# Optimization experiments

Hardware: AMD Instinct MI355X
Metric: run time of the kernel (lower is better)

Reference implementation:

```python
import jax, jax.numpy as jnp
import numpy as np

T, M = 8192, 64  # timesteps, number of correlated series


def setup_inputs() -> dict:
    key = jax.random.key(0)
    k_y, k_mu, k_sig = jax.random.split(key, 3)
    y = jax.random.normal(k_y, (T, M), dtype=jnp.float32)
    MU = (jax.random.normal(k_mu, (M,), dtype=jnp.float32) * 0.01)
    sigma0 = jax.random.uniform(k_sig, (M,), dtype=jnp.float32, minval=0.5, maxval=1.5)
    alpha0 = sigma0  # ctor initializes alpha0 = std(y,0) as well
    alpha = jnp.full((M,), 0.25, dtype=jnp.float32)
    beta = jnp.full((M,), 0.25, dtype=jnp.float32)
    # L0 = cholesky of a correlation matrix (ctor uses corrcoef(y.T))
    rng = np.random.default_rng(0)
    Z = rng.standard_normal((M, 4 * M)).astype(np.float64)
    C = Z @ Z.T
    d = np.sqrt(np.diag(C))
    C = C / np.outer(d, d)
    L0 = jnp.asarray(np.linalg.cholesky(C), dtype=jnp.float32)
    A = jnp.full((1,), 0.9, dtype=jnp.float32)
    B = jnp.full((1,), 0.05, dtype=jnp.float32)
    return dict(y=y, MU=MU, sigma0=sigma0, alpha0=alpha0, alpha=alpha,
                beta=beta, L0=L0, A=A, B=B)


def reference(y, MU, sigma0, alpha0, alpha, beta, L0, A, B):
    """DCC-GARCH conditional moments.
    Returns (mus [T,M], Sigmas [T,M,M]) — the parameters of the
    MultivariateNormalFullCovariance the TF model constructs.
    """
    n = y.shape[1]
    A0 = L0.T @ L0                  # unconditional correlation target (M,M)
    a0 = alpha0 ** 2                # (M,)

    def step(carry, y_t):
        u, sig, Q = carry           # u:(M,), sig:(M,), Q:(M,M)
        sig_t = jnp.sqrt(a0 + alpha * sig ** 2 + beta * u ** 2)
        ustd = u / sig
        Psi = jnp.outer(ustd, ustd)
        Q_t = A0 + A * (Q - A0) + B * (Psi - A0)
        dinv = 1.0 / jnp.sqrt(jnp.diagonal(Q_t))
        R_t = Q_t * jnp.outer(dinv, dinv)        # cov_to_corr
        Sigma_t = R_t * jnp.outer(sig_t, sig_t)  # D_t @ R_t @ D_t
        return (y_t - MU, sig_t, Q_t), Sigma_t

    u0 = jnp.zeros((n,), dtype=y.dtype)
    _, Sigmas = jax.lax.scan(step, (u0, sigma0, A0), y)
    mus = jnp.broadcast_to(MU, y.shape)
    return mus, Sigmas
```

## Files before the change

kernel.cpp:

```cpp
#include <hip/hip_runtime.h>
#include <hip/hip_bf16.h>
#include <stdint.h>

#define TT 8192
#define MM 64
#define CHUNK 32
#define WQ 48
#define WS 16
#define YROWS (CHUNK + WQ + WS)
#define NSPLIT 4

typedef float f4 __attribute__((ext_vector_type(4)));

__global__ __launch_bounds__(256, 4)
void dcc_kernel(const float* __restrict__ y, const float* __restrict__ MU,
                const float* __restrict__ sigma0, const float* __restrict__ alpha0,
                const float* __restrict__ alpha, const float* __restrict__ beta,
                const float* __restrict__ L0, const float* __restrict__ Ap,
                const float* __restrict__ Bp,
                float* __restrict__ out)
{
    __shared__ float lds_yu[YROWS][MM];
    __shared__ float lds_s[CHUNK][MM];

    const int tid  = threadIdx.x;
    const int chnk = blockIdx.x >> 2;
    const int h    = blockIdx.x & 3;
    const int c0   = chnk * CHUNK;
    const int cend = c0 + CHUNK;
    const int tq0  = (c0 > WQ) ? (c0 - WQ) : 0;
    const int ts0  = (tq0 > WS) ? (tq0 - WS) : 0;

    const float A = Ap[0], B = Bp[0];
    const float kappa = 1.0f - A - B;

    float* out_mu = out;
    float* out_sg = out + (size_t)TT * MM;

    if (h == 0) {
        int o = tid * 8;
        int m = o & (MM - 1);
        f4 a = *(const f4*)(MU + m);
        f4 b = *(const f4*)(MU + m + 4);
        float* dst = out_mu + (size_t)c0 * MM + o;
        __builtin_nontemporal_store(a, (f4*)(dst));
        __builtin_nontemporal_store(b, (f4*)(dst + 4));
    }

    {
        const float* ysrc = y + (size_t)ts0 * MM;
        const int nflt = (cend - ts0) * MM;
        for (int o = tid * 4; o < nflt; o += 256 * 4) {
            f4 v = *(const f4*)(ysrc + o);
            *(f4*)(&lds_yu[0][0] + o) = v;
        }
    }
    __syncthreads();

    if (tid < MM) {
        const int m = tid;
        const float mu  = MU[m];
        const float al  = alpha[m], be = beta[m];
        const float a0v = alpha0[m] * alpha0[m];
        float s2 = sigma0[m] * sigma0[m];
        float u_prev = (ts0 > 0) ? (y[(size_t)(ts0 - 1) * MM + m] - mu) : 0.0f;
        for (int t = ts0; t < cend; ++t) {
            float yt  = lds_yu[t - ts0][m];
            float s2n = fmaf(al, s2, fmaf(be, u_prev * u_prev, a0v));
            if (t >= tq0) lds_yu[t - tq0][m] = u_prev * rsqrtf(s2);
            if (t >= c0)  lds_s[t - c0][m]   = sqrtf(s2n);
            u_prev = yt - mu;
            s2 = s2n;
        }
    }

    const int j0 = (tid & 15) * 4;
    const int i0 = h * 16 + (tid >> 4);

    float acc[4], adr = 0.f, adc[4];
    #pragma unroll
    for (int b = 0; b < 4; ++b) { acc[b] = 0.f; adc[b] = 0.f; }

    #pragma unroll 4
    for (int k = 0; k < MM; ++k) {
        float li = L0[k * MM + i0];
        f4 Lj = *(const f4*)(L0 + k * MM + j0);
        float lj[4] = {Lj.x, Lj.y, Lj.z, Lj.w};
        #pragma unroll
        for (int b = 0; b < 4; ++b) {
            acc[b] = fmaf(li, lj[b], acc[b]);
            adc[b] = fmaf(lj[b], lj[b], adc[b]);
        }
        adr = fmaf(li, li, adr);
    }
    __syncthreads();

    float q[4], Cm[4], qdc[4], Cdc[4];
    float qdr = adr, Cdr = kappa * adr;
    #pragma unroll
    for (int b = 0; b < 4; ++b) {
        q[b]   = acc[b];
        Cm[b]  = kappa * acc[b];
        qdc[b] = adc[b];
        Cdc[b] = kappa * adc[b];
    }

    for (int t = tq0; t < cend; ++t) {
        const int r = t - tq0;
        float ui = lds_yu[r][i0];
        f4 U_j = *(const f4*)(&lds_yu[r][j0]);
        float uj[4] = {U_j.x, U_j.y, U_j.z, U_j.w};
        float bui = B * ui;
        #pragma unroll
        for (int b = 0; b < 4; ++b) {
            q[b] = fmaf(A, q[b], fmaf(bui, uj[b], Cm[b]));
            float buj = B * uj[b];
            qdc[b] = fmaf(A, qdc[b], fmaf(buj, uj[b], Cdc[b]));
        }
        qdr = fmaf(A, qdr, fmaf(bui, ui, Cdr));
        if (t >= c0) {
            float si = lds_s[t - c0][i0];
            f4 S_j = *(const f4*)(&lds_s[t - c0][j0]);
            float f = si * rsqrtf(qdr);
            float rj[4] = { S_j.x * rsqrtf(qdc[0]), S_j.y * rsqrtf(qdc[1]),
                            S_j.z * rsqrtf(qdc[2]), S_j.w * rsqrtf(qdc[3]) };
            f4 w;
            w.x = q[0] * f * rj[0];
            w.y = q[1] * f * rj[1];
            w.z = q[2] * f * rj[2];
            w.w = q[3] * f * rj[3];
            float* o = out_sg + ((size_t)t << 12) + (i0 << 6) + j0;
            __builtin_nontemporal_store(w, (f4*)o);
        }
    }
}

extern "C" void kernel_launch(void* const* d_in, const int* in_sizes, int n_in,
                              void* d_out, int out_size, void* d_ws, size_t ws_size,
                              hipStream_t stream) {
    (void)in_sizes; (void)n_in; (void)out_size; (void)d_ws; (void)ws_size;
    const float* y      = (const float*)d_in[0];
    const float* MU     = (const float*)d_in[1];
    const float* sigma0 = (const float*)d_in[2];
    const float* alpha0 = (const float*)d_in[3];
    const float* alpha  = (const float*)d_in[4];
    const float* beta   = (const float*)d_in[5];
    const float* L0     = (const float*)d_in[6];
    const float* A      = (const float*)d_in[7];
    const float* B      = (const float*)d_in[8];
    dcc_kernel<<<dim3((TT / CHUNK) * NSPLIT), dim3(256), 0, stream>>>(
        y, MU, sigma0, alpha0, alpha, beta, L0, A, B, (float*)d_out);
}
```

Measured before the change: 180.5 us.

## Split DCC into state kernel and output kernel via workspace buffers

Splits the single fused kernel into two launches. The first computes per-series standardized residuals and a combined scale factor (sigma times the inverse sqrt of the Q diagonal) into workspace, plus L0^T L0 once. The second recomputes only the off-diagonal Q recurrence per chunk and writes Sigma. This removes the redundant 4x recomputation of the variance scan, the L0 product and the diagonal Q recurrences in every block, and doubles the chunk size to amortize warm-up. In exchange it adds a second launch, workspace round-trips, and switches from nontemporal to regular stores.

```diff
diff --git a/kernel.cpp b/kernel.cpp
--- a/kernel.cpp
+++ b/kernel.cpp
@@ -1,59 +1,76 @@
 #include <hip/hip_runtime.h>
-#include <hip/hip_bf16.h>
 #include <stdint.h>
 
 #define TT 8192
 #define MM 64
-#define CHUNK 32
-#define WQ 48
-#define WS 16
-#define YROWS (CHUNK + WQ + WS)
+#define ACH 32
+#define AWQ 48
+#define AWS 16
+#define AROWS (ACH + AWQ + AWS)
+#define BCH 64
+#define BWQ 48
+#define BROWS (BCH + BWQ)
 #define NSPLIT 4
 
 typedef float f4 __attribute__((ext_vector_type(4)));
 
-__global__ __launch_bounds__(256, 4)
-void dcc_kernel(const float* __restrict__ y, const float* __restrict__ MU,
-                const float* __restrict__ sigma0, const float* __restrict__ alpha0,
-                const float* __restrict__ alpha, const float* __restrict__ beta,
-                const float* __restrict__ L0, const float* __restrict__ Ap,
-                const float* __restrict__ Bp,
-                float* __restrict__ out)
+__global__ __launch_bounds__(256, 2)
+void dcc_state(const float* __restrict__ y, const float* __restrict__ MU,
+               const float* __restrict__ sigma0, const float* __restrict__ alpha0,
+               const float* __restrict__ alpha, const float* __restrict__ beta,
+               const float* __restrict__ L0, const float* __restrict__ Ap,
+               const float* __restrict__ Bp,
+               float* __restrict__ out_mu, float* __restrict__ ustd_ws,
+               float* __restrict__ g_ws, float* __restrict__ a0_ws)
 {
-    __shared__ float lds_yu[YROWS][MM];
-    __shared__ float lds_s[CHUNK][MM];
-
-    const int tid  = threadIdx.x;
-    const int chnk = blockIdx.x >> 2;
-    const int h    = blockIdx.x & 3;
-    const int c0   = chnk * CHUNK;
-    const int cend = c0 + CHUNK;
-    const int tq0  = (c0 > WQ) ? (c0 - WQ) : 0;
-    const int ts0  = (tq0 > WS) ? (tq0 - WS) : 0;
-
+    const int tid = threadIdx.x;
+    const int blk = blockIdx.x;
     const float A = Ap[0], B = Bp[0];
     const float kappa = 1.0f - A - B;
 
-    float* out_mu = out;
-    float* out_sg = out + (size_t)TT * MM;
-
-    if (h == 0) {
+    if (blk == TT / ACH) {
+        const int i  = tid >> 2;
+        const int j0 = (tid & 3) * 16;
+        float acc[16];
+        #pragma unroll
+        for (int b = 0; b < 16; ++b) acc[b] = 0.f;
+        for (int k = 0; k < MM; ++k) {
+            float li = L0[k * MM + i];
+            const float* row = L0 + k * MM + j0;
+            #pragma unroll
+            for (int b = 0; b < 16; ++b)
+                acc[b] = fmaf(li, row[b], acc[b]);
+        }
+        #pragma unroll
+        for (int b = 0; b < 16; b += 4) {
+            f4 w = {acc[b], acc[b + 1], acc[b + 2], acc[b + 3]};
+            *(f4*)(a0_ws + i * MM + j0 + b) = w;
+        }
+        return;
+    }
+
+    __shared__ float lds_y[AROWS][MM];
+
+    const int c0   = blk * ACH;
+    const int cend = c0 + ACH;
+    const int tq0  = (c0 > AWQ) ? c0 - AWQ : 0;
+    const int ts0  = (tq0 > AWS) ? tq0 - AWS : 0;
+
+    {
         int o = tid * 8;
         int m = o & (MM - 1);
         f4 a = *(const f4*)(MU + m);
         f4 b = *(const f4*)(MU + m + 4);
         float* dst = out_mu + (size_t)c0 * MM + o;
-        __builtin_nontemporal_store(a, (f4*)(dst));
-        __builtin_nontemporal_store(b, (f4*)(dst + 4));
+        *(f4*)dst       = a;
+        *(f4*)(dst + 4) = b;
     }
 
     {
         const float* ysrc = y + (size_t)ts0 * MM;
         const int nflt = (cend - ts0) * MM;
-        for (int o = tid * 4; o < nflt; o += 256 * 4) {
-            f4 v = *(const f4*)(ysrc + o);
-            *(f4*)(&lds_yu[0][0] + o) = v;
-        }
+        for (int o = tid * 4; o < nflt; o += 1024)
+            *(f4*)(&lds_y[0][0] + o) = *(const f4*)(ysrc + o);
     }
     __syncthreads();
 
@@ -62,83 +79,104 @@
         const float mu  = MU[m];
         const float al  = alpha[m], be = beta[m];
         const float a0v = alpha0[m] * alpha0[m];
+        float adm = 0.f;
+        for (int k = 0; k < MM; ++k) {
+            float l = L0[k * MM + m];
+            adm = fmaf(l, l, adm);
+        }
+        const float Cd = kappa * adm;
+        float qd = adm;
         float s2 = sigma0[m] * sigma0[m];
         float u_prev = (ts0 > 0) ? (y[(size_t)(ts0 - 1) * MM + m] - mu) : 0.0f;
         for (int t = ts0; t < cend; ++t) {
-            float yt  = lds_yu[t - ts0][m];
+            float yt  = lds_y[t - ts0][m];
             float s2n = fmaf(al, s2, fmaf(be, u_prev * u_prev, a0v));
-            if (t >= tq0) lds_yu[t - tq0][m] = u_prev * rsqrtf(s2);
-            if (t >= c0)  lds_s[t - c0][m]   = sqrtf(s2n);
+            float us  = u_prev * rsqrtf(s2);
+            if (t >= tq0) qd = fmaf(A, qd, fmaf(B * us, us, Cd));
+            if (t >= c0) {
+                ustd_ws[(size_t)t * MM + m] = us;
+                g_ws[(size_t)t * MM + m]    = sqrtf(s2n) * rsqrtf(qd);
+            }
             u_prev = yt - mu;
             s2 = s2n;
         }
     }
-
+}
+
+__global__ __launch_bounds__(256, 2)
+void dcc_out(const float* __restrict__ ustd_ws, const float* __restrict__ g_ws,
+             const float* __restrict__ a0_ws, const float* __restrict__ Ap,
+             const float* __restrict__ Bp, float* __restrict__ out_sg)
+{
+    __shared__ float lds_u[BROWS][MM];
+    __shared__ float lds_g[BCH][MM];
+
+    const int tid  = threadIdx.x;
+    const int chnk = blockIdx.x >> 2;
+    const int h    = blockIdx.x & 3;
+    const int c0   = chnk * BCH;
+    const int tq0  = (c0 > BWQ) ? c0 - BWQ : 0;
+    const int wn   = c0 - tq0;
+    const float A = Ap[0], B = Bp[0];
+    const float kappa = 1.0f - A - B;
+
+    {
+        const float* usrc = ustd_ws + (size_t)tq0 * MM;
+        const int nflt = (wn + BCH) * MM;
+        for (int o = tid * 4; o < nflt; o += 1024)
+            *(f4*)(&lds_u[0][0] + o) = *(const f4*)(usrc + o);
+        const float* gsrc = g_ws + (size_t)c0 * MM;
+        #pragma unroll
+        for (int o0 = 0; o0 < BCH * MM; o0 += 1024)
+            *(f4*)(&lds_g[0][0] + o0 + tid * 4) = *(const f4*)(gsrc + o0 + tid * 4);
+    }
+    __syncthreads();
+
+    const int i0 = h * 16 + (tid >> 4);
     const int j0 = (tid & 15) * 4;
-    const int i0 = h * 16 + (tid >> 4);
-
-    float acc[4], adr = 0.f, adc[4];
-    #pragma unroll
-    for (int b = 0; b < 4; ++b) { acc[b] = 0.f; adc[b] = 0.f; }
+
+    f4 a0 = *(const f4*)(a0_ws + i0 * MM + j0);
+    float q[4]  = {a0.x, a0.y, a0.z, a0.w};
+    float Cm[4] = {kappa * q[0], kappa * q[1], kappa * q[2], kappa * q[3]};
 
     #pragma unroll 4
-    for (int k = 0; k < MM; ++k) {
-        float li = L0[k * MM + i0];
-        f4 Lj = *(const f4*)(L0 + k * MM + j0);
-        float lj[4] = {Lj.x, Lj.y, Lj.z, Lj.w};
-        #pragma unroll
-        for (int b = 0; b < 4; ++b) {
-            acc[b] = fmaf(li, lj[b], acc[b]);
-            adc[b] = fmaf(lj[b], lj[b], adc[b]);
-        }
-        adr = fmaf(li, li, adr);
-    }
-    __syncthreads();
-
-    float q[4], Cm[4], qdc[4], Cdc[4];
-    float qdr = adr, Cdr = kappa * adr;
-    #pragma unroll
-    for (int b = 0; b < 4; ++b) {
-        q[b]   = acc[b];
-        Cm[b]  = kappa * acc[b];
-        qdc[b] = adc[b];
-        Cdc[b] = kappa * adc[b];
-    }
-
-    for (int t = tq0; t < cend; ++t) {
-        const int r = t - tq0;
-        float ui = lds_yu[r][i0];
-        f4 U_j = *(const f4*)(&lds_yu[r][j0]);
-        float uj[4] = {U_j.x, U_j.y, U_j.z, U_j.w};
+    for (int r = 0; r < wn; ++r) {
+        float ui = lds_u[r][i0];
+        f4   uj  = *(const f4*)(&lds_u[r][j0]);
         float bui = B * ui;
-        #pragma unroll
-        for (int b = 0; b < 4; ++b) {
-            q[b] = fmaf(A, q[b], fmaf(bui, uj[b], Cm[b]));
-            float buj = B * uj[b];
-            qdc[b] = fmaf(A, qdc[b], fmaf(buj, uj[b], Cdc[b]));
-        }
-        qdr = fmaf(A, qdr, fmaf(bui, ui, Cdr));
-        if (t >= c0) {
-            float si = lds_s[t - c0][i0];
-            f4 S_j = *(const f4*)(&lds_s[t - c0][j0]);
-            float f = si * rsqrtf(qdr);
-            float rj[4] = { S_j.x * rsqrtf(qdc[0]), S_j.y * rsqrtf(qdc[1]),
-                            S_j.z * rsqrtf(qdc[2]), S_j.w * rsqrtf(qdc[3]) };
-            f4 w;
-            w.x = q[0] * f * rj[0];
-            w.y = q[1] * f * rj[1];
-            w.z = q[2] * f * rj[2];
-            w.w = q[3] * f * rj[3];
-            float* o = out_sg + ((size_t)t << 12) + (i0 << 6) + j0;
-            __builtin_nontemporal_store(w, (f4*)o);
-        }
+        q[0] = fmaf(A, q[0], fmaf(bui, uj.x, Cm[0]));
+        q[1] = fmaf(A, q[1], fmaf(bui, uj.y, Cm[1]));
+        q[2] = fmaf(A, q[2], fmaf(bui, uj.z, Cm[2]));
+        q[3] = fmaf(A, q[3], fmaf(bui, uj.w, Cm[3]));
+    }
+
+    float* obase = out_sg + ((size_t)c0 << 12) + (i0 << 6) + j0;
+    #pragma unroll 4
+    for (int r2 = 0; r2 < BCH; ++r2) {
+        int r = wn + r2;
+        float ui = lds_u[r][i0];
+        f4   uj  = *(const f4*)(&lds_u[r][j0]);
+        float bui = B * ui;
+        q[0] = fmaf(A, q[0], fmaf(bui, uj.x, Cm[0]));
+        q[1] = fmaf(A, q[1], fmaf(bui, uj.y, Cm[1]));
+        q[2] = fmaf(A, q[2], fmaf(bui, uj.z, Cm[2]));
+        q[3] = fmaf(A, q[3], fmaf(bui, uj.w, Cm[3]));
+        float gi = lds_g[r2][i0];
+        f4   gj  = *(const f4*)(&lds_g[r2][j0]);
+        float fgi = gi;
+        f4 w;
+        w.x = q[0] * fgi * gj.x;
+        w.y = q[1] * fgi * gj.y;
+        w.z = q[2] * fgi * gj.z;
+        w.w = q[3] * fgi * gj.w;
+        *(f4*)(obase + ((size_t)r2 << 12)) = w;
     }
 }
 
 extern "C" void kernel_launch(void* const* d_in, const int* in_sizes, int n_in,
                               void* d_out, int out_size, void* d_ws, size_t ws_size,
                               hipStream_t stream) {
-    (void)in_sizes; (void)n_in; (void)out_size; (void)d_ws; (void)ws_size;
+    (void)in_sizes; (void)n_in; (void)out_size; (void)ws_size;
     const float* y      = (const float*)d_in[0];
     const float* MU     = (const float*)d_in[1];
     const float* sigma0 = (const float*)d_in[2];
@@ -148,6 +186,18 @@
     const float* L0     = (const float*)d_in[6];
     const float* A      = (const float*)d_in[7];
     const float* B      = (const float*)d_in[8];
-    dcc_kernel<<<dim3((TT / CHUNK) * NSPLIT), dim3(256), 0, stream>>>(
-        y, MU, sigma0, alpha0, alpha, beta, L0, A, B, (float*)d_out);
+
+    float* out_mu = (float*)d_out;
+    float* out_sg = out_mu + (size_t)TT * MM;
+
+    float* ws      = (float*)d_ws;
+    float* ustd_ws = ws;
+    float* g_ws    = ws + (size_t)TT * MM;
+    float* a0_ws   = ws + 2 * (size_t)TT * MM;
+
+    dcc_state<<<dim3(TT / ACH + 1), dim3(256), 0, stream>>>(
+        y, MU, sigma0, alpha0, alpha, beta, L0, A, B,
+        out_mu, ustd_ws, g_ws, a0_ws);
+    dcc_out<<<dim3((TT / BCH) * NSPLIT), dim3(256), 0, stream>>>(
+        ustd_ws, g_ws, a0_ws, A, B, out_sg);
 }
```

Result: faster. 175.9 us (-2.6%).
